# Kernel tuning notes

Measured on AMD Instinct MI355X. Metric: run time of the kernel, lower is better.

## Reference

```python
import jax, jax.numpy as jnp
import numpy as np

N = 100000          # total nodes across batched graphs
E = 1600000         # total edges (avg degree 16)
D = 64              # in_dim == hidden_dim == out_dim
L = 3               # num_layers
EPS = 1e-5          # LayerNorm eps


def setup_inputs() -> dict:
    key = jax.random.key(0)
    ks = jax.random.split(key, 7)
    features = jax.random.normal(ks[0], (N, D), dtype=jnp.float32)
    src = jax.random.randint(ks[1], (E,), 0, N, dtype=jnp.int32)
    dst = jax.random.randint(ks[2], (E,), 0, N, dtype=jnp.int32)
    # MRConv linear: concat([x_i, max_j(x_j - x_i)]) @ W + b, per layer
    Ws = jax.random.normal(ks[3], (L, 2 * D, D), dtype=jnp.float32) / np.sqrt(2 * D)
    bs = jnp.zeros((L, D), dtype=jnp.float32)
    gammas = jnp.ones((L, D), dtype=jnp.float32)
    betas = jnp.zeros((L, D), dtype=jnp.float32)
    return dict(features=features, src=src, dst=dst, Ws=Ws, bs=bs,
                gammas=gammas, betas=betas)


def _layer_norm(h, gamma, beta):
    mu = jnp.mean(h, axis=-1, keepdims=True)
    var = jnp.mean(jnp.square(h - mu), axis=-1, keepdims=True)
    return (h - mu) * jax.lax.rsqrt(var + EPS) * gamma + beta


def reference(features, src, dst, Ws, bs, gammas, betas):
    x = features
    for l in range(L):
        # MRConv message: x_src - x_dst, max-aggregated at dst.
        rel = x[src] - x[dst]                                   # [E, D]
        agg = jax.ops.segment_max(rel, dst, num_segments=N)      # [N, D]
        # self-loop (added per graph in the original) contributes 0 to the max;
        # also fixes -inf for nodes with no incoming edges
        agg = jnp.maximum(agg, 0.0)
        h = jnp.concatenate([x, agg], axis=-1) @ Ws[l] + bs[l]   # [N, D]
        h = _layer_norm(h, gammas[l], betas[l])
        x = jax.nn.elu(h)
    # original returns the re-batched graph with updated node features
    return x
```

## Files before the change

kernel.cpp:

```cpp
#include <hip/hip_runtime.h>
#include <hip/hip_bf16.h>
#include <math.h>

#define N_NODES 100000
#define N_EDGES 1600000
#define D 64
#define TWO_D 128
#define LN_EPS 1e-5f

#define BSHIFT 7
#define BMASK 127
#define NBUCK ((N_NODES + 127) >> BSHIFT)
#define BCAP 4096
#define EPB 8192
#define NEB ((N_EDGES + EPB - 1) / EPB)
#define BOFS_STRIDE (NBUCK + 1)
#define NTILES ((N_NODES + 63) / 64)
#define XQ (N_NODES * D / 4)
#define WELEMS (3 * 4 * 4 * 64 * 8)

typedef __attribute__((ext_vector_type(4))) float f32x4;
typedef __attribute__((ext_vector_type(8))) _Float16 h16x8;
typedef __attribute__((ext_vector_type(8))) unsigned short u16x8;

__device__ __forceinline__ unsigned short f2h(float f) {
    return __builtin_bit_cast(unsigned short, (_Float16)f);
}
__device__ __forceinline__ u16x8 pkmaxh(u16x8 a, u16x8 b) {
    return __builtin_bit_cast(u16x8,
        __builtin_elementwise_max(__builtin_bit_cast(h16x8, a),
                                  __builtin_bit_cast(h16x8, b)));
}

__global__ __launch_bounds__(1024) void bscat_kernel(const int* __restrict__ src,
                                                     const int* __restrict__ dst,
                                                     int* __restrict__ ebuf,
                                                     int* __restrict__ bofs) {
    __shared__ int cnt[NBUCK];
    __shared__ int off[NBUCK];
    __shared__ int stage[EPB];
    const int e0 = blockIdx.x * EPB;
    const int nE = min(EPB, N_EDGES - e0);
    int d[8], s[8];

    for (int i = threadIdx.x; i < NBUCK; i += 1024) cnt[i] = 0;
    __syncthreads();
#pragma unroll
    for (int k = 0; k < 8; ++k) {
        const int i = threadIdx.x + k * 1024;
        if (i < nE) {
            d[k] = dst[e0 + i];
            s[k] = src[e0 + i];
            atomicAdd(&cnt[d[k] >> BSHIFT], 1);
        }
    }
    __syncthreads();
    const int v = (threadIdx.x < NBUCK) ? cnt[threadIdx.x] : 0;
    if (threadIdx.x < NBUCK) off[threadIdx.x] = v;
    __syncthreads();
    for (int o = 1; o < 1024; o <<= 1) {
        int t = 0;
        if (threadIdx.x < NBUCK && threadIdx.x >= o) t = off[threadIdx.x - o];
        __syncthreads();
        if (threadIdx.x < NBUCK) off[threadIdx.x] += t;
        __syncthreads();
    }
    if (threadIdx.x < NBUCK) {
        const int ex = off[threadIdx.x] - v;
        bofs[blockIdx.x * BOFS_STRIDE + threadIdx.x] = ex;
        off[threadIdx.x] = ex;
        cnt[threadIdx.x] = 0;
    }
    if (threadIdx.x == 0) bofs[blockIdx.x * BOFS_STRIDE + NBUCK] = nE;
    __syncthreads();
#pragma unroll
    for (int k = 0; k < 8; ++k) {
        const int i = threadIdx.x + k * 1024;
        if (i < nE) {
            const int b = d[k] >> BSHIFT;
            const int r = atomicAdd(&cnt[b], 1);
            stage[off[b] + r] = (s[k] << BSHIFT) | (d[k] & BMASK);
        }
    }
    __syncthreads();
    for (int i = threadIdx.x; i < nE; i += 1024)
        ebuf[e0 + i] = stage[i];
}

__global__ __launch_bounds__(512) void bbuild_kernel(const int* __restrict__ ebuf,
                                                     const int* __restrict__ bofs,
                                                     int* __restrict__ row_ptr,
                                                     int* __restrict__ deg,
                                                     int* __restrict__ ssrc,
                                                     ushort* __restrict__ pairs) {
    __shared__ int rst[NEB], rlen[NEB], rdst[NEB];
    __shared__ int stage[BCAP];
    __shared__ int stage2[BCAP];
    __shared__ int cnt[128], excl[128];
    const int b = blockIdx.x;
    const int nb0 = b << BSHIFT;

    for (int i = threadIdx.x; i < NEB; i += 512) {
        const int st = bofs[i * BOFS_STRIDE + b];
        const int en = bofs[i * BOFS_STRIDE + b + 1];
        rst[i] = st; rlen[i] = en - st;
    }
    __syncthreads();
    const int rv = (threadIdx.x < NEB) ? rlen[threadIdx.x] : 0;
    if (threadIdx.x < NEB) rdst[threadIdx.x] = rv;
    __syncthreads();
    for (int o = 1; o < 256; o <<= 1) {
        int t = 0;
        if (threadIdx.x < NEB && threadIdx.x >= o) t = rdst[threadIdx.x - o];
        __syncthreads();
        if (threadIdx.x < NEB) rdst[threadIdx.x] += t;
        __syncthreads();
    }
    const int total = rdst[NEB - 1];

    for (int pos = threadIdx.x; pos < total; pos += 512) {
        int lo = 0, hi = NEB - 1;
        while (lo < hi) {
            const int mid = (lo + hi) >> 1;
            if (rdst[mid] <= pos) lo = mid + 1; else hi = mid;
        }
        const int doff = rdst[lo] - rlen[lo];
        stage[pos] = ebuf[lo * EPB + rst[lo] + (pos - doff)];
    }
    if (threadIdx.x < 128) cnt[threadIdx.x] = 0;
    __syncthreads();

    for (int i = threadIdx.x; i < total; i += 512)
        atomicAdd(&cnt[stage[i] & BMASK], 1);
    __syncthreads();
    const int cv = (threadIdx.x < 128) ? cnt[threadIdx.x] : 0;
    if (threadIdx.x < 128) excl[threadIdx.x] = cv;
    __syncthreads();
    for (int o = 1; o < 128; o <<= 1) {
        int t = 0;
        if (threadIdx.x < 128 && threadIdx.x >= o) t = excl[threadIdx.x - o];
        __syncthreads();
        if (threadIdx.x < 128) excl[threadIdx.x] += t;
        __syncthreads();
    }
    const int lane = threadIdx.x & 63;
    if (threadIdx.x < 128) {
        excl[threadIdx.x] -= cv;
        const int node = nb0 + threadIdx.x;
        if (node < N_NODES) {
            row_ptr[node] = b * BCAP + excl[threadIdx.x];
            deg[node] = cv;
        }
        cnt[threadIdx.x] = 0;
    }

    if (threadIdx.x < 128) {
        const int tile = 2 * b + (threadIdx.x >> 6);
        if (tile < NTILES) {
            int key = (cv << 6) | lane;
#pragma unroll
            for (int k = 2; k <= 64; k <<= 1) {
#pragma unroll
                for (int jj = k >> 1; jj > 0; jj >>= 1) {
                    const int other = __shfl_xor(key, jj, 64);
                    const bool up = ((lane & k) == 0);
                    const bool lower = ((lane & jj) == 0);
                    key = (lower == up) ? min(key, other) : max(key, other);
                }
            }
            const int small_nl = key & 63;
            const int big_nl = __shfl(key, 63 - lane, 64) & 63;
            if (lane < 32)
                pairs[tile * 32 + lane] = (ushort)((big_nl << 6) | small_nl);
        }
    }
    __syncthreads();

    for (int i = threadIdx.x; i < total; i += 512) {
        const int p = stage[i];
        const int dl = p & BMASK;
        const int r = atomicAdd(&cnt[dl], 1);
        stage2[excl[dl] + r] = p >> BSHIFT;
    }
    __syncthreads();
    for (int i = threadIdx.x; i < total; i += 512)
        ssrc[b * BCAP + i] = stage2[i];
}

__global__ __launch_bounds__(256) void cvt_kernel(const float* __restrict__ xf,
                                                  const float* __restrict__ Ws,
                                                  ushort* __restrict__ xb,
                                                  ushort* __restrict__ Wperm) {
    int i = blockIdx.x * 256 + threadIdx.x;
    if (i < XQ) {
        float4 v = ((const float4*)xf)[i];
        ushort4 o;
        o.x = f2h(v.x); o.y = f2h(v.y); o.z = f2h(v.z); o.w = f2h(v.w);
        ((ushort4*)xb)[i] = o;
    } else {
        int k = i - XQ;
        if (k < WELEMS) {
            int j    = k & 7;
            int lane = (k >> 3) & 63;
            int c    = (k >> 9) & 3;
            int s    = (k >> 11) & 3;
            int lay  = k >> 13;
            int kk = 32 * s + 8 * (lane >> 4) + j;
            int dd = 16 * c + (lane & 15);
            Wperm[k] = f2h(Ws[((size_t)lay * TWO_D + kk) * D + dd]);
        }
    }
}

__device__ __forceinline__ void gather_node(const u16x8* __restrict__ x8,
                                            const int* __restrict__ ssrc,
                                            int fl, int base, int beg, int end,
                                            u16x8& m) {
    if (beg >= end) return;
    int j = beg;
    int cnt = min(end - j, 8);
    int idx = ssrc[j + min(fl, cnt - 1)];

    int s0 = __shfl(idx, base, 64);
    int s1 = __shfl(idx, base + min(1, cnt - 1), 64);
    int s2 = __shfl(idx, base + min(2, cnt - 1), 64);
    int s3 = __shfl(idx, base + min(3, cnt - 1), 64);
    u16x8 a0 = x8[s0 * 8 + fl];
    u16x8 a1 = x8[s1 * 8 + fl];
    u16x8 a2 = x8[s2 * 8 + fl];
    u16x8 a3 = x8[s3 * 8 + fl];

    while (true) {
        int s4 = __shfl(idx, base + min(4, cnt - 1), 64);
        int s5 = __shfl(idx, base + min(5, cnt - 1), 64);
        int s6 = __shfl(idx, base + min(6, cnt - 1), 64);
        int s7 = __shfl(idx, base + min(7, cnt - 1), 64);
        u16x8 b0 = x8[s4 * 8 + fl];
        u16x8 b1 = x8[s5 * 8 + fl];
        u16x8 b2 = x8[s6 * 8 + fl];
        u16x8 b3 = x8[s7 * 8 + fl];

        const int nj = j + cnt;
        const bool more = nj < end;
        int ncnt = cnt, nidx = idx;
        if (more) {
            ncnt = min(end - nj, 8);
            nidx = ssrc[nj + min(fl, ncnt - 1)];
        }

        m = pkmaxh(m, pkmaxh(pkmaxh(a0, a1), pkmaxh(a2, a3)));

        if (more) {
            int u0 = __shfl(nidx, base, 64);
            int u1 = __shfl(nidx, base + min(1, ncnt - 1), 64);
            int u2 = __shfl(nidx, base + min(2, ncnt - 1), 64);
            int u3 = __shfl(nidx, base + min(3, ncnt - 1), 64);
            a0 = x8[u0 * 8 + fl];
            a1 = x8[u1 * 8 + fl];
            a2 = x8[u2 * 8 + fl];
            a3 = x8[u3 * 8 + fl];
        }

        m = pkmaxh(m, pkmaxh(pkmaxh(b0, b1), pkmaxh(b2, b3)));

        if (!more) break;
        j = nj; cnt = ncnt; idx = nidx;
    }
}

__global__ __launch_bounds__(256, 8) void layer_kernel(
    const ushort* __restrict__ xb,
    const int* __restrict__ row_ptr,
    const int* __restrict__ deg,
    const int* __restrict__ ssrc,
    const ushort* __restrict__ pairs,
    const ushort* __restrict__ Wperm,
    const float* __restrict__ bias,
    const float* __restrict__ gamma,
    const float* __restrict__ beta,
    ushort* __restrict__ out_b,
    float*  __restrict__ out_f)
{
    __shared__ u16x8 xt[64][8];
    __shared__ u16x8 at[64][8];

    const int tid = threadIdx.x;
    const int fl = tid & 7;
    const int base = tid & 56;
    const int grp = tid >> 3;
    const u16x8* __restrict__ x8 = (const u16x8*)xb;
    const int nblk0 = blockIdx.x * 64;

    const int pr = pairs[blockIdx.x * 32 + grp];
    const int nls[2] = { pr & 63, (pr >> 6) & 63 };

#pragma unroll
    for (int q = 0; q < 2; ++q) {
        const int nl = nls[q];
        const int node = nblk0 + nl;
        if (node < N_NODES) {
            const int beg = row_ptr[node];
            const int end = beg + deg[node];

            u16x8 m;
#pragma unroll
            for (int e = 0; e < 8; ++e) m[e] = 0xFC00;
            gather_node(x8, ssrc, fl, base, beg, end, m);

            const u16x8 xs = x8[node * 8 + fl];
            u16x8 o;
            if (end > beg) {
                h16x8 dd = __builtin_bit_cast(h16x8, m) -
                           __builtin_bit_cast(h16x8, xs);
                h16x8 zz = 0;
                o = __builtin_bit_cast(u16x8, __builtin_elementwise_max(dd, zz));
            } else {
#pragma unroll
                for (int e = 0; e < 8; ++e) o[e] = 0;
            }
            const int slot = fl ^ (nl & 7);
            xt[nl][slot] = xs;
            at[nl][slot] = o;
        }
    }
    __syncthreads();

    const int wave = tid >> 6;
    const int lane = tid & 63;
    const int n0 = nblk0 + wave * 16;
    if (n0 >= N_NODES) return;
    const int row = lane & 15;
    const int kb  = lane >> 4;
    const int nl  = wave * 16 + row;
    const int sw  = nl & 7;

    h16x8 a0 = __builtin_bit_cast(h16x8, xt[nl][kb ^ sw]);
    h16x8 a1 = __builtin_bit_cast(h16x8, xt[nl][(kb + 4) ^ sw]);
    h16x8 a2 = __builtin_bit_cast(h16x8, at[nl][kb ^ sw]);
    h16x8 a3 = __builtin_bit_cast(h16x8, at[nl][(kb + 4) ^ sw]);

    const h16x8* __restrict__ wp = (const h16x8*)Wperm;
    h16x8 wf[4][4];
#pragma unroll
    for (int s = 0; s < 4; ++s)
#pragma unroll
        for (int c = 0; c < 4; ++c)
            wf[s][c] = wp[(s * 4 + c) * 64 + lane];

    f32x4 acc[4];
#pragma unroll
    for (int c = 0; c < 4; ++c) acc[c] = (f32x4){0.f, 0.f, 0.f, 0.f};
#pragma unroll
    for (int c = 0; c < 4; ++c) {
        acc[c] = __builtin_amdgcn_mfma_f32_16x16x32_f16(a0, wf[0][c], acc[c], 0, 0, 0);
        acc[c] = __builtin_amdgcn_mfma_f32_16x16x32_f16(a1, wf[1][c], acc[c], 0, 0, 0);
        acc[c] = __builtin_amdgcn_mfma_f32_16x16x32_f16(a2, wf[2][c], acc[c], 0, 0, 0);
        acc[c] = __builtin_amdgcn_mfma_f32_16x16x32_f16(a3, wf[3][c], acc[c], 0, 0, 0);
    }

    float bv[4], gv[4], btv[4];
#pragma unroll
    for (int c = 0; c < 4; ++c) {
        const int col = 16 * c + row;
        bv[c] = bias[col]; gv[c] = gamma[col]; btv[c] = beta[col];
    }

#pragma unroll
    for (int j = 0; j < 4; ++j) {
        float h0 = acc[0][j] + bv[0];
        float h1 = acc[1][j] + bv[1];
        float h2 = acc[2][j] + bv[2];
        float h3 = acc[3][j] + bv[3];
        float ps = (h0 + h1) + (h2 + h3);
        ps += __shfl_xor(ps, 1, 64);
        ps += __shfl_xor(ps, 2, 64);
        ps += __shfl_xor(ps, 4, 64);
        ps += __shfl_xor(ps, 8, 64);
        const float mu = ps * (1.0f / 64.0f);
        const float d0 = h0 - mu, d1 = h1 - mu, d2 = h2 - mu, d3 = h3 - mu;
        float vs = (d0 * d0 + d1 * d1) + (d2 * d2 + d3 * d3);
        vs += __shfl_xor(vs, 1, 64);
        vs += __shfl_xor(vs, 2, 64);
        vs += __shfl_xor(vs, 4, 64);
        vs += __shfl_xor(vs, 8, 64);
        const float rstd = rsqrtf(vs * (1.0f / 64.0f) + LN_EPS);

        const int node = n0 + 4 * kb + j;
        const float dd[4] = {d0, d1, d2, d3};
#pragma unroll
        for (int c = 0; c < 4; ++c) {
            float o = dd[c] * rstd * gv[c] + btv[c];
            o = o > 0.f ? o : expm1f(o);
            if (out_f) out_f[node * D + 16 * c + row] = o;
            else       out_b[node * D + 16 * c + row] = f2h(o);
        }
    }
}

static inline size_t alignup(size_t v) { return (v + 255) & ~(size_t)255; }

extern "C" void kernel_launch(void* const* d_in, const int* in_sizes, int n_in,
                              void* d_out, int out_size, void* d_ws, size_t ws_size,
                              hipStream_t stream) {
    const float* features = (const float*)d_in[0];
    const int*   src      = (const int*)d_in[1];
    const int*   dst      = (const int*)d_in[2];
    const float* Ws       = (const float*)d_in[3];
    const float* bs       = (const float*)d_in[4];
    const float* gammas   = (const float*)d_in[5];
    const float* betas    = (const float*)d_in[6];
    float* out = (float*)d_out;

    char* ws = (char*)d_ws;
    size_t off = 0;
    int* row_ptr = (int*)(ws + off); off = alignup(off + sizeof(int) * N_NODES);
    int* deg     = (int*)(ws + off); off = alignup(off + sizeof(int) * N_NODES);
    int* bofs    = (int*)(ws + off); off = alignup(off + sizeof(int) * (size_t)NEB * BOFS_STRIDE);
    int* ebuf    = (int*)(ws + off); off = alignup(off + sizeof(int) * (size_t)NEB * EPB);
    int* ssrc    = (int*)(ws + off); off = alignup(off + sizeof(int) * (size_t)NBUCK * BCAP);
    ushort* prs  = (ushort*)(ws + off); off = alignup(off + sizeof(ushort) * (size_t)NTILES * 32);
    ushort* xbA  = (ushort*)(ws + off); off = alignup(off + sizeof(ushort) * (size_t)N_NODES * D);
    ushort* xbB  = (ushort*)(ws + off); off = alignup(off + sizeof(ushort) * (size_t)N_NODES * D);
    ushort* Wperm= (ushort*)(ws + off); off = alignup(off + sizeof(ushort) * 3 * TWO_D * D);

    bscat_kernel<<<NEB, 1024, 0, stream>>>(src, dst, ebuf, bofs);
    bbuild_kernel<<<NBUCK, 512, 0, stream>>>(ebuf, bofs, row_ptr, deg, ssrc, prs);

    cvt_kernel<<<(XQ + WELEMS + 255) / 256, 256, 0, stream>>>(features, Ws, xbA, Wperm);

    ushort* xin = xbA;
    ushort* xnb[3] = { xbB, xbA, nullptr };
    for (int l = 0; l < 3; ++l) {
        layer_kernel<<<NTILES, 256, 0, stream>>>(
            xin, row_ptr, deg, ssrc, prs,
            Wperm + (size_t)l * 16 * 64 * 8,
            bs + (size_t)l * D,
            gammas + (size_t)l * D,
            betas + (size_t)l * D,
            xnb[l],
            (l == 2) ? out : nullptr);
        xin = xnb[l];
    }
}
```

Before: 140.8 us.

## Fuse conversion into bucket scatter, halve edge chunk, pipeline paired-node gathers

Merges the feature/weight fp16 conversion kernel into the edge bucket-scatter kernel as extra blocks, removing one launch and letting the two independent jobs run concurrently. Halves the edges per scatter block so twice as many blocks spread across the GPU, and widens the bbuild prefix scan to cover the larger block count. In the layer kernel, the two nodes handled by each 8-lane group are now gathered in one continuous software-pipelined stream, so the first loads for the second node are issued while the first node is still being reduced. This adds branch and index logic, and the bbuild kernel must now merge twice as many runs per bucket.

```diff
diff --git a/kernel.cpp b/kernel.cpp
--- a/kernel.cpp
+++ b/kernel.cpp
@@ -12,12 +12,13 @@
 #define BMASK 127
 #define NBUCK ((N_NODES + 127) >> BSHIFT)
 #define BCAP 4096
-#define EPB 8192
+#define EPB 4096
 #define NEB ((N_EDGES + EPB - 1) / EPB)
 #define BOFS_STRIDE (NBUCK + 1)
 #define NTILES ((N_NODES + 63) / 64)
 #define XQ (N_NODES * D / 4)
 #define WELEMS (3 * 4 * 4 * 64 * 8)
+#define CVT_BLOCKS ((XQ + WELEMS + 1023) / 1024)
 
 typedef __attribute__((ext_vector_type(4))) float f32x4;
 typedef __attribute__((ext_vector_type(8))) _Float16 h16x8;
@@ -32,59 +33,85 @@
                                   __builtin_bit_cast(h16x8, b)));
 }
 
-__global__ __launch_bounds__(1024) void bscat_kernel(const int* __restrict__ src,
+__global__ __launch_bounds__(1024) void setup_kernel(const int* __restrict__ src,
                                                      const int* __restrict__ dst,
                                                      int* __restrict__ ebuf,
-                                                     int* __restrict__ bofs) {
-    __shared__ int cnt[NBUCK];
-    __shared__ int off[NBUCK];
-    __shared__ int stage[EPB];
-    const int e0 = blockIdx.x * EPB;
-    const int nE = min(EPB, N_EDGES - e0);
-    int d[8], s[8];
-
-    for (int i = threadIdx.x; i < NBUCK; i += 1024) cnt[i] = 0;
-    __syncthreads();
-#pragma unroll
-    for (int k = 0; k < 8; ++k) {
-        const int i = threadIdx.x + k * 1024;
-        if (i < nE) {
-            d[k] = dst[e0 + i];
-            s[k] = src[e0 + i];
-            atomicAdd(&cnt[d[k] >> BSHIFT], 1);
-        }
-    }
-    __syncthreads();
-    const int v = (threadIdx.x < NBUCK) ? cnt[threadIdx.x] : 0;
-    if (threadIdx.x < NBUCK) off[threadIdx.x] = v;
-    __syncthreads();
-    for (int o = 1; o < 1024; o <<= 1) {
-        int t = 0;
-        if (threadIdx.x < NBUCK && threadIdx.x >= o) t = off[threadIdx.x - o];
-        __syncthreads();
-        if (threadIdx.x < NBUCK) off[threadIdx.x] += t;
-        __syncthreads();
-    }
-    if (threadIdx.x < NBUCK) {
-        const int ex = off[threadIdx.x] - v;
-        bofs[blockIdx.x * BOFS_STRIDE + threadIdx.x] = ex;
-        off[threadIdx.x] = ex;
-        cnt[threadIdx.x] = 0;
-    }
-    if (threadIdx.x == 0) bofs[blockIdx.x * BOFS_STRIDE + NBUCK] = nE;
-    __syncthreads();
-#pragma unroll
-    for (int k = 0; k < 8; ++k) {
-        const int i = threadIdx.x + k * 1024;
-        if (i < nE) {
-            const int b = d[k] >> BSHIFT;
-            const int r = atomicAdd(&cnt[b], 1);
-            stage[off[b] + r] = (s[k] << BSHIFT) | (d[k] & BMASK);
-        }
-    }
-    __syncthreads();
-    for (int i = threadIdx.x; i < nE; i += 1024)
-        ebuf[e0 + i] = stage[i];
+                                                     int* __restrict__ bofs,
+                                                     const float* __restrict__ xf,
+                                                     const float* __restrict__ Ws,
+                                                     ushort* __restrict__ xb,
+                                                     ushort* __restrict__ Wperm) {
+    if (blockIdx.x < NEB) {
+        __shared__ int cnt[NBUCK];
+        __shared__ int off[NBUCK];
+        __shared__ int stage[EPB];
+        const int e0 = blockIdx.x * EPB;
+        const int nE = min(EPB, N_EDGES - e0);
+        int d[4], s[4];
+
+        for (int i = threadIdx.x; i < NBUCK; i += 1024) cnt[i] = 0;
+        __syncthreads();
+#pragma unroll
+        for (int k = 0; k < 4; ++k) {
+            const int i = threadIdx.x + k * 1024;
+            if (i < nE) {
+                d[k] = dst[e0 + i];
+                s[k] = src[e0 + i];
+                atomicAdd(&cnt[d[k] >> BSHIFT], 1);
+            }
+        }
+        __syncthreads();
+        const int v = (threadIdx.x < NBUCK) ? cnt[threadIdx.x] : 0;
+        if (threadIdx.x < NBUCK) off[threadIdx.x] = v;
+        __syncthreads();
+        for (int o = 1; o < 1024; o <<= 1) {
+            int t = 0;
+            if (threadIdx.x < NBUCK && threadIdx.x >= o) t = off[threadIdx.x - o];
+            __syncthreads();
+            if (threadIdx.x < NBUCK) off[threadIdx.x] += t;
+            __syncthreads();
+        }
+        if (threadIdx.x < NBUCK) {
+            const int ex = off[threadIdx.x] - v;
+            bofs[blockIdx.x * BOFS_STRIDE + threadIdx.x] = ex;
+            off[threadIdx.x] = ex;
+            cnt[threadIdx.x] = 0;
+        }
+        if (threadIdx.x == 0) bofs[blockIdx.x * BOFS_STRIDE + NBUCK] = nE;
+        __syncthreads();
+#pragma unroll
+        for (int k = 0; k < 4; ++k) {
+            const int i = threadIdx.x + k * 1024;
+            if (i < nE) {
+                const int b = d[k] >> BSHIFT;
+                const int r = atomicAdd(&cnt[b], 1);
+                stage[off[b] + r] = (s[k] << BSHIFT) | (d[k] & BMASK);
+            }
+        }
+        __syncthreads();
+        for (int i = threadIdx.x; i < nE; i += 1024)
+            ebuf[e0 + i] = stage[i];
+    } else {
+        const int i = (blockIdx.x - NEB) * 1024 + threadIdx.x;
+        if (i < XQ) {
+            float4 v = ((const float4*)xf)[i];
+            ushort4 o;
+            o.x = f2h(v.x); o.y = f2h(v.y); o.z = f2h(v.z); o.w = f2h(v.w);
+            ((ushort4*)xb)[i] = o;
+        } else {
+            const int k = i - XQ;
+            if (k < WELEMS) {
+                int j    = k & 7;
+                int lane = (k >> 3) & 63;
+                int c    = (k >> 9) & 3;
+                int s    = (k >> 11) & 3;
+                int lay  = k >> 13;
+                int kk = 32 * s + 8 * (lane >> 4) + j;
+                int dd = 16 * c + (lane & 15);
+                Wperm[k] = f2h(Ws[((size_t)lay * TWO_D + kk) * D + dd]);
+            }
+        }
+    }
 }
 
 __global__ __launch_bounds__(512) void bbuild_kernel(const int* __restrict__ ebuf,
@@ -109,7 +136,7 @@
     const int rv = (threadIdx.x < NEB) ? rlen[threadIdx.x] : 0;
     if (threadIdx.x < NEB) rdst[threadIdx.x] = rv;
     __syncthreads();
-    for (int o = 1; o < 256; o <<= 1) {
+    for (int o = 1; o < 512; o <<= 1) {
         int t = 0;
         if (threadIdx.x < NEB && threadIdx.x >= o) t = rdst[threadIdx.x - o];
         __syncthreads();
@@ -187,84 +214,102 @@
         ssrc[b * BCAP + i] = stage2[i];
 }
 
-__global__ __launch_bounds__(256) void cvt_kernel(const float* __restrict__ xf,
-                                                  const float* __restrict__ Ws,
-                                                  ushort* __restrict__ xb,
-                                                  ushort* __restrict__ Wperm) {
-    int i = blockIdx.x * 256 + threadIdx.x;
-    if (i < XQ) {
-        float4 v = ((const float4*)xf)[i];
-        ushort4 o;
-        o.x = f2h(v.x); o.y = f2h(v.y); o.z = f2h(v.z); o.w = f2h(v.w);
-        ((ushort4*)xb)[i] = o;
-    } else {
-        int k = i - XQ;
-        if (k < WELEMS) {
-            int j    = k & 7;
-            int lane = (k >> 3) & 63;
-            int c    = (k >> 9) & 3;
-            int s    = (k >> 11) & 3;
-            int lay  = k >> 13;
-            int kk = 32 * s + 8 * (lane >> 4) + j;
-            int dd = 16 * c + (lane & 15);
-            Wperm[k] = f2h(Ws[((size_t)lay * TWO_D + kk) * D + dd]);
-        }
-    }
-}
-
-__device__ __forceinline__ void gather_node(const u16x8* __restrict__ x8,
+__device__ __forceinline__ void gather_pair(const u16x8* __restrict__ x8,
                                             const int* __restrict__ ssrc,
-                                            int fl, int base, int beg, int end,
-                                            u16x8& m) {
-    if (beg >= end) return;
-    int j = beg;
-    int cnt = min(end - j, 8);
-    int idx = ssrc[j + min(fl, cnt - 1)];
-
-    int s0 = __shfl(idx, base, 64);
-    int s1 = __shfl(idx, base + min(1, cnt - 1), 64);
-    int s2 = __shfl(idx, base + min(2, cnt - 1), 64);
-    int s3 = __shfl(idx, base + min(3, cnt - 1), 64);
-    u16x8 a0 = x8[s0 * 8 + fl];
-    u16x8 a1 = x8[s1 * 8 + fl];
-    u16x8 a2 = x8[s2 * 8 + fl];
-    u16x8 a3 = x8[s3 * 8 + fl];
-
-    while (true) {
-        int s4 = __shfl(idx, base + min(4, cnt - 1), 64);
-        int s5 = __shfl(idx, base + min(5, cnt - 1), 64);
-        int s6 = __shfl(idx, base + min(6, cnt - 1), 64);
-        int s7 = __shfl(idx, base + min(7, cnt - 1), 64);
-        u16x8 b0 = x8[s4 * 8 + fl];
-        u16x8 b1 = x8[s5 * 8 + fl];
-        u16x8 b2 = x8[s6 * 8 + fl];
-        u16x8 b3 = x8[s7 * 8 + fl];
-
-        const int nj = j + cnt;
-        const bool more = nj < end;
-        int ncnt = cnt, nidx = idx;
-        if (more) {
-            ncnt = min(end - nj, 8);
-            nidx = ssrc[nj + min(fl, ncnt - 1)];
-        }
-
-        m = pkmaxh(m, pkmaxh(pkmaxh(a0, a1), pkmaxh(a2, a3)));
-
-        if (more) {
-            int u0 = __shfl(nidx, base, 64);
-            int u1 = __shfl(nidx, base + min(1, ncnt - 1), 64);
-            int u2 = __shfl(nidx, base + min(2, ncnt - 1), 64);
-            int u3 = __shfl(nidx, base + min(3, ncnt - 1), 64);
-            a0 = x8[u0 * 8 + fl];
-            a1 = x8[u1 * 8 + fl];
-            a2 = x8[u2 * 8 + fl];
-            a3 = x8[u3 * 8 + fl];
-        }
-
-        m = pkmaxh(m, pkmaxh(pkmaxh(b0, b1), pkmaxh(b2, b3)));
-
-        if (!more) break;
-        j = nj; cnt = ncnt; idx = nidx;
+                                            int fl, int base,
+                                            int begA, int dA, int begB, int dB,
+                                            u16x8& mA, u16x8& mB)
+{
+    const int total = dA + dB;
+    if (total <= 0) return;
+
+    int j = 0;
+    int cnt = (dA > 0) ? min(8, dA) : min(8, total);
+    {
+        const int v = j + min(fl, cnt - 1);
+        const int p = (v < dA) ? begA + v : begB + (v - dA);
+        int idx = ssrc[p];
+
+        int s0 = __shfl(idx, base, 64);
+        int s1 = __shfl(idx, base + min(1, cnt - 1), 64);
+        int s2 = __shfl(idx, base + min(2, cnt - 1), 64);
+        int s3 = __shfl(idx, base + min(3, cnt - 1), 64);
+        u16x8 a0 = x8[s0 * 8 + fl];
+        u16x8 a1 = x8[s1 * 8 + fl];
+        u16x8 a2 = x8[s2 * 8 + fl];
+        u16x8 a3 = x8[s3 * 8 + fl];
+
+        while (j < dA) {
+            int s4 = __shfl(idx, base + min(4, cnt - 1), 64);
+            int s5 = __shfl(idx, base + min(5, cnt - 1), 64);
+            int s6 = __shfl(idx, base + min(6, cnt - 1), 64);
+            int s7 = __shfl(idx, base + min(7, cnt - 1), 64);
+            u16x8 b0 = x8[s4 * 8 + fl];
+            u16x8 b1 = x8[s5 * 8 + fl];
+            u16x8 b2 = x8[s6 * 8 + fl];
+            u16x8 b3 = x8[s7 * 8 + fl];
+
+            const int nj = j + cnt;
+            const bool more = nj < total;
+            int ncnt = cnt, nidx = idx;
+            if (more) {
+                ncnt = (nj < dA) ? min(8, dA - nj) : min(8, total - nj);
+                const int nv = nj + min(fl, ncnt - 1);
+                nidx = ssrc[(nv < dA) ? begA + nv : begB + (nv - dA)];
+            }
+
+            mA = pkmaxh(mA, pkmaxh(pkmaxh(a0, a1), pkmaxh(a2, a3)));
+
+            if (more) {
+                int u0 = __shfl(nidx, base, 64);
+                int u1 = __shfl(nidx, base + min(1, ncnt - 1), 64);
+                int u2 = __shfl(nidx, base + min(2, ncnt - 1), 64);
+                int u3 = __shfl(nidx, base + min(3, ncnt - 1), 64);
+                a0 = x8[u0 * 8 + fl];
+                a1 = x8[u1 * 8 + fl];
+                a2 = x8[u2 * 8 + fl];
+                a3 = x8[u3 * 8 + fl];
+            }
+
+            mA = pkmaxh(mA, pkmaxh(pkmaxh(b0, b1), pkmaxh(b2, b3)));
+            j = nj; cnt = ncnt; idx = nidx;
+        }
+
+        while (j < total) {
+            int s4 = __shfl(idx, base + min(4, cnt - 1), 64);
+            int s5 = __shfl(idx, base + min(5, cnt - 1), 64);
+            int s6 = __shfl(idx, base + min(6, cnt - 1), 64);
+            int s7 = __shfl(idx, base + min(7, cnt - 1), 64);
+            u16x8 b0 = x8[s4 * 8 + fl];
+            u16x8 b1 = x8[s5 * 8 + fl];
+            u16x8 b2 = x8[s6 * 8 + fl];
+            u16x8 b3 = x8[s7 * 8 + fl];
+
+            const int nj = j + cnt;
+            const bool more = nj < total;
+            int ncnt = cnt, nidx = idx;
+            if (more) {
+                ncnt = min(8, total - nj);
+                const int nv = nj + min(fl, ncnt - 1);
+                nidx = ssrc[begB + (nv - dA)];
+            }
+
+            mB = pkmaxh(mB, pkmaxh(pkmaxh(a0, a1), pkmaxh(a2, a3)));
+
+            if (more) {
+                int u0 = __shfl(nidx, base, 64);
+                int u1 = __shfl(nidx, base + min(1, ncnt - 1), 64);
+                int u2 = __shfl(nidx, base + min(2, ncnt - 1), 64);
+                int u3 = __shfl(nidx, base + min(3, ncnt - 1), 64);
+                a0 = x8[u0 * 8 + fl];
+                a1 = x8[u1 * 8 + fl];
+                a2 = x8[u2 * 8 + fl];
+                a3 = x8[u3 * 8 + fl];
+            }
+
+            mB = pkmaxh(mB, pkmaxh(pkmaxh(b0, b1), pkmaxh(b2, b3)));
+            j = nj; cnt = ncnt; idx = nidx;
+        }
     }
 }
 
@@ -292,36 +337,48 @@
     const int nblk0 = blockIdx.x * 64;
 
     const int pr = pairs[blockIdx.x * 32 + grp];
-    const int nls[2] = { pr & 63, (pr >> 6) & 63 };
-
-#pragma unroll
-    for (int q = 0; q < 2; ++q) {
-        const int nl = nls[q];
-        const int node = nblk0 + nl;
-        if (node < N_NODES) {
-            const int beg = row_ptr[node];
-            const int end = beg + deg[node];
-
-            u16x8 m;
-#pragma unroll
-            for (int e = 0; e < 8; ++e) m[e] = 0xFC00;
-            gather_node(x8, ssrc, fl, base, beg, end, m);
-
-            const u16x8 xs = x8[node * 8 + fl];
-            u16x8 o;
-            if (end > beg) {
-                h16x8 dd = __builtin_bit_cast(h16x8, m) -
-                           __builtin_bit_cast(h16x8, xs);
-                h16x8 zz = 0;
-                o = __builtin_bit_cast(u16x8, __builtin_elementwise_max(dd, zz));
-            } else {
-#pragma unroll
-                for (int e = 0; e < 8; ++e) o[e] = 0;
-            }
-            const int slot = fl ^ (nl & 7);
-            xt[nl][slot] = xs;
-            at[nl][slot] = o;
-        }
+    const int nlA = pr & 63, nlB = (pr >> 6) & 63;
+    const int nodeA = nblk0 + nlA, nodeB = nblk0 + nlB;
+    const bool vA = nodeA < N_NODES, vB = nodeB < N_NODES;
+
+    int begA = 0, dA = 0, begB = 0, dB = 0;
+    if (vA) { begA = row_ptr[nodeA]; dA = deg[nodeA]; }
+    if (vB) { begB = row_ptr[nodeB]; dB = deg[nodeB]; }
+
+    u16x8 mA, mB;
+#pragma unroll
+    for (int e = 0; e < 8; ++e) { mA[e] = 0xFC00; mB[e] = 0xFC00; }
+    gather_pair(x8, ssrc, fl, base, begA, dA, begB, dB, mA, mB);
+
+    if (vA) {
+        const u16x8 xs = x8[nodeA * 8 + fl];
+        u16x8 o;
+        if (dA > 0) {
+            h16x8 dd = __builtin_bit_cast(h16x8, mA) - __builtin_bit_cast(h16x8, xs);
+            h16x8 zz = 0;
+            o = __builtin_bit_cast(u16x8, __builtin_elementwise_max(dd, zz));
+        } else {
+#pragma unroll
+            for (int e = 0; e < 8; ++e) o[e] = 0;
+        }
+        const int slot = fl ^ (nlA & 7);
+        xt[nlA][slot] = xs;
+        at[nlA][slot] = o;
+    }
+    if (vB) {
+        const u16x8 xs = x8[nodeB * 8 + fl];
+        u16x8 o;
+        if (dB > 0) {
+            h16x8 dd = __builtin_bit_cast(h16x8, mB) - __builtin_bit_cast(h16x8, xs);
+            h16x8 zz = 0;
+            o = __builtin_bit_cast(u16x8, __builtin_elementwise_max(dd, zz));
+        } else {
+#pragma unroll
+            for (int e = 0; e < 8; ++e) o[e] = 0;
+        }
+        const int slot = fl ^ (nlB & 7);
+        xt[nlB][slot] = xs;
+        at[nlB][slot] = o;
     }
     __syncthreads();
 
@@ -423,10 +480,9 @@
     ushort* xbB  = (ushort*)(ws + off); off = alignup(off + sizeof(ushort) * (size_t)N_NODES * D);
     ushort* Wperm= (ushort*)(ws + off); off = alignup(off + sizeof(ushort) * 3 * TWO_D * D);
 
-    bscat_kernel<<<NEB, 1024, 0, stream>>>(src, dst, ebuf, bofs);
+    setup_kernel<<<NEB + CVT_BLOCKS, 1024, 0, stream>>>(src, dst, ebuf, bofs,
+                                                        features, Ws, xbA, Wperm);
     bbuild_kernel<<<NBUCK, 512, 0, stream>>>(ebuf, bofs, row_ptr, deg, ssrc, prs);
-
-    cvt_kernel<<<(XQ + WELEMS + 255) / 256, 256, 0, stream>>>(features, Ws, xbA, Wperm);
 
     ushort* xin = xbA;
     ushort* xnb[3] = { xbB, xbA, nullptr };
```

New measurement: 182.3 us. 29.5% more time.
